# Kernel optimization log

Measured on AMD Instinct MI355X. Metric: run time of the kernel, lower is better.

Reference implementation:

```python
import jax, jax.numpy as jnp
import numpy as np

E, K, IN_DIM, OUT_DIM = 100000, 16, 128, 128


def _linear_init(key, out_d, in_d):
    kw, kb = jax.random.split(key)
    bound = 1.0 / np.sqrt(in_d)
    W = jax.random.uniform(kw, (out_d, in_d), minval=-bound, maxval=bound, dtype=jnp.float32)
    b = jax.random.uniform(kb, (out_d,), minval=-bound, maxval=bound, dtype=jnp.float32)
    return W, b


def setup_inputs() -> dict:
    key = jax.random.key(0)
    k_feat, k_adj, k1, k2, k3, k4 = jax.random.split(key, 6)
    edge_features = jax.random.normal(k_feat, (E, IN_DIM), dtype=jnp.float32)
    edge_adjacency = jax.random.randint(k_adj, (E, K), 0, E, dtype=jnp.int64)
    mW1, mb1 = _linear_init(k1, OUT_DIM, 2 * IN_DIM)
    mW2, mb2 = _linear_init(k2, OUT_DIM, OUT_DIM)
    uW1, ub1 = _linear_init(k3, OUT_DIM, IN_DIM + OUT_DIM)
    uW2, ub2 = _linear_init(k4, OUT_DIM, OUT_DIM)
    return {"edge_features": edge_features, "edge_adjacency": edge_adjacency,
            "mW1": mW1, "mb1": mb1, "mW2": mW2, "mb2": mb2,
            "uW1": uW1, "ub1": ub1, "uW2": ub2 * 0 + ub2 if False else uW1 * 0 + uW1 if False else uW1, "ub1_": ub1} if False else {
            "edge_features": edge_features, "edge_adjacency": edge_adjacency,
            "mW1": mW1, "mb1": mb1, "mW2": mW2, "mb2": mb2,
            "uW1": uW1, "ub1": ub1, "uW2": uW2, "ub2": ub2}


def reference(edge_features, edge_adjacency, mW1, mb1, mW2, mb2, uW1, ub1, uW2, ub2):
    D = edge_features.shape[1]
    # message_net first Linear on concat([feat_i, feat_j]) split into two halves
    # to avoid materializing the [E, K, 2D] concat tensor.
    Wi, Wj = mW1[:, :D], mW1[:, D:]                      # each [O, D]
    self_part = edge_features @ Wi.T                     # [E, O]
    nbr_feat = edge_features[edge_adjacency]             # [E, K, D] gather
    h = jax.nn.relu(self_part[:, None, :] + jnp.einsum('ekd,od->eko', nbr_feat, Wj) + mb1)
    msg = jnp.einsum('eko,po->ekp', h, mW2) + mb2        # [E, K, O]
    msg = msg.mean(axis=1)                               # mean over neighbors -> [E, O]
    # update_net on concat([feat_i, msg_i]), split likewise
    Ui, Um = uW1[:, :D], uW1[:, D:]
    u = jax.nn.relu(edge_features @ Ui.T + msg @ Um.T + ub1)
    return u @ uW2.T + ub2                               # [E, O]
```

## Files before the change

### kernel.cpp

```cpp
#include <hip/hip_runtime.h>
#include <hip/hip_bf16.h>

#define NE 100000
#define NK 16
#define ND 128
#define NTILES 6250
#define NSUP 3125

typedef __bf16 bf16_t;
typedef bf16_t bf16x8 __attribute__((ext_vector_type(8)));
typedef bf16_t bf16x4 __attribute__((ext_vector_type(4)));
typedef float f32x4 __attribute__((ext_vector_type(4)));
typedef float f32x2 __attribute__((ext_vector_type(2)));
typedef unsigned u32x2 __attribute__((ext_vector_type(2)));
typedef unsigned short u16;
typedef unsigned char u8;

__device__ __forceinline__ u16 f2bf(float f) {
  bf16_t h = (bf16_t)f;
  return __builtin_bit_cast(u16, h);
}

__device__ __forceinline__ void soft_barrier() {
  asm volatile("s_waitcnt lgkmcnt(0)" ::: "memory");
  __builtin_amdgcn_s_barrier();
}

__device__ __forceinline__ void unpack_s(unsigned w0, unsigned w1,
                                         f32x4& sA, f32x4& sB) {
  const f32x2 a0 = __builtin_amdgcn_cvt_pk_f32_fp8(w0, false);
  const f32x2 a1 = __builtin_amdgcn_cvt_pk_f32_fp8(w0, true);
  const f32x2 a2 = __builtin_amdgcn_cvt_pk_f32_fp8(w1, false);
  const f32x2 a3 = __builtin_amdgcn_cvt_pk_f32_fp8(w1, true);
  sA[0] = a0[0]; sA[1] = a0[1]; sA[2] = a1[0]; sA[3] = a1[1];
  sB[0] = a2[0]; sB[1] = a2[1]; sB[2] = a3[0]; sB[3] = a3[1];
}

__device__ __forceinline__ void acc8(f32x4& hA, f32x4& hB,
                                     const f32x4 sA, const f32x4 sB,
                                     const u32x2 zw) {
  const f32x2 z0 = __builtin_amdgcn_cvt_pk_f32_fp8(zw[0], false);
  const f32x2 z1 = __builtin_amdgcn_cvt_pk_f32_fp8(zw[0], true);
  const f32x2 z2 = __builtin_amdgcn_cvt_pk_f32_fp8(zw[1], false);
  const f32x2 z3 = __builtin_amdgcn_cvt_pk_f32_fp8(zw[1], true);
  f32x4 vA = sA, vB = sB;
  vA[0] += z0[0]; vA[1] += z0[1]; vA[2] += z1[0]; vA[3] += z1[1];
  vB[0] += z2[0]; vB[1] += z2[1]; vB[2] += z3[0]; vB[3] += z3[1];
#pragma unroll
  for (int i = 0; i < 4; ++i) {
    vA[i] = fmaxf(vA[i], 0.f);
    vB[i] = fmaxf(vB[i], 0.f);
  }
  hA += vA;
  hB += vB;
}

__global__ void k_prep(const float* __restrict__ mW1, const float* __restrict__ uW1,
                       const float* __restrict__ uW2, const float* __restrict__ mW2,
                       const float* __restrict__ ub1, const float* __restrict__ mb2,
                       u16* __restrict__ Wi_b, u16* __restrict__ Wj_b,
                       u16* __restrict__ Ui_b, u16* __restrict__ Wp_b,
                       u16* __restrict__ W2_b, float* __restrict__ bp)
{
  const int o = blockIdx.x, t = threadIdx.x;
  Wi_b[o * ND + t] = f2bf(mW1[o * 256 + t]);
  Wj_b[o * ND + t] = f2bf(mW1[o * 256 + 128 + t]);
  Ui_b[o * ND + t] = f2bf(uW1[o * 256 + t]);
  W2_b[o * ND + t] = f2bf(uW2[o * ND + t]);
  float acc = 0.f;
  for (int p = 0; p < 128; ++p)
    acc += uW1[o * 256 + 128 + p] * mW2[p * 128 + t];
  Wp_b[o * ND + t] = f2bf(acc);
  if (t == 0) {
    float b = ub1[o];
    for (int p = 0; p < 128; ++p) b += uW1[o * 256 + 128 + p] * mb2[p];
    bp[o] = b;
  }
}

__global__ __launch_bounds__(512) void k1_szt(
    const float* __restrict__ X, const u16* __restrict__ Wi_b,
    const u16* __restrict__ Wj_b, const u16* __restrict__ Ui_b,
    const float* __restrict__ mb1, const float* __restrict__ bp,
    u8* __restrict__ Sf8, u8* __restrict__ Zf8, u16* __restrict__ Tp)
{
  __shared__ u16 xt[2][16 * ND];
  __shared__ u8  eS[2][16 * ND];
  __shared__ u8  eZ[2][16 * ND];
  __shared__ u16 eT[2][16 * ND];
  const int tid = threadIdx.x, wid = tid >> 6, lane = tid & 63;
  const int r = lane & 15, q = lane >> 4;

  bf16x8 wiF[4], wjF[4], uiF[4];
  f32x4 mbF, bpF;
  {
    const int row = wid * 16 + r;
#pragma unroll
    for (int kk = 0; kk < 4; ++kk) {
      wiF[kk] = *(const bf16x8*)(Wi_b + row * ND + kk * 32 + q * 8);
      wjF[kk] = *(const bf16x8*)(Wj_b + row * ND + kk * 32 + q * 8);
      uiF[kk] = *(const bf16x8*)(Ui_b + row * ND + kk * 32 + q * 8);
    }
    mbF = *(const f32x4*)(mb1 + wid * 16 + q * 4);
    bpF = *(const f32x4*)(bp  + wid * 16 + q * 4);
  }

  const int rs = tid >> 5, cs = tid & 31;
  const int stb = rs * 256 + ((((cs >> 1) ^ (rs & 15)) << 4) | ((cs & 1) << 3));
  const int ewb = r * 256 + ((((wid * 2 + (q >> 1)) ^ (r & 15)) << 4) | ((q & 1) << 3));
  const int ezb = r * 128 + (((wid ^ (r & 7)) << 4) | (q * 4));
  const int erow = tid >> 5, c8 = tid & 31;
  const int erb = erow * 256 + ((((c8 >> 1) ^ (erow & 15)) << 4) | ((c8 & 1) << 3));
  const int zrb = erow * 128 + ((((c8 >> 2) ^ (erow & 7)) << 4) | ((c8 & 3) << 2));

  const long stride = gridDim.x;
  long t = blockIdx.x;
  if (t >= NTILES) return;

  f32x4 xr;
  auto gload = [&](long tt) {
    xr = *(const f32x4*)(X + (tt * 16 + rs) * ND + cs * 4);
  };
  auto stage = [&](int bb) {
    bf16x4 b;
#pragma unroll
    for (int i = 0; i < 4; ++i) b[i] = (bf16_t)xr[i];
    *(bf16x4*)((char*)xt[bb] + stb) = b;
  };

  gload(t);
  stage(0);
  {
    const long t1 = t + stride;
    if (t1 < NTILES) gload(t1);
  }
  soft_barrier();
  int b = 0;

  for (; t < NTILES; t += stride) {
    const long tn = t + stride, tn2 = tn + stride;

    bf16x8 xf[4];
#pragma unroll
    for (int kk = 0; kk < 4; ++kk)
      xf[kk] = *(const bf16x8*)((const char*)xt[b] +
               r * 256 + (((kk * 4 + q) ^ (r & 15)) << 4));

    if (tn < NTILES) stage(b ^ 1);
    if (tn2 < NTILES) gload(tn2);

    f32x4 aS = {0.f, 0.f, 0.f, 0.f};
    f32x4 aZ = {0.f, 0.f, 0.f, 0.f};
    f32x4 aT = {0.f, 0.f, 0.f, 0.f};
#pragma unroll
    for (int kk = 0; kk < 4; ++kk) {
      aS = __builtin_amdgcn_mfma_f32_16x16x32_bf16(wiF[kk], xf[kk], aS, 0, 0, 0);
      aZ = __builtin_amdgcn_mfma_f32_16x16x32_bf16(wjF[kk], xf[kk], aZ, 0, 0, 0);
      aT = __builtin_amdgcn_mfma_f32_16x16x32_bf16(uiF[kk], xf[kk], aT, 0, 0, 0);
    }

    bf16x4 pT;
#pragma unroll
    for (int i = 0; i < 4; ++i) pT[i] = (bf16_t)(aT[i] + bpF[i]);
    unsigned spk = 0, zpk = 0;
    spk = __builtin_amdgcn_cvt_pk_fp8_f32(aS[0] + mbF[0], aS[1] + mbF[1], spk, false);
    spk = __builtin_amdgcn_cvt_pk_fp8_f32(aS[2] + mbF[2], aS[3] + mbF[3], spk, true);
    zpk = __builtin_amdgcn_cvt_pk_fp8_f32(aZ[0], aZ[1], zpk, false);
    zpk = __builtin_amdgcn_cvt_pk_fp8_f32(aZ[2], aZ[3], zpk, true);
    *(unsigned*)((char*)eS[b] + ezb) = spk;
    *(unsigned*)((char*)eZ[b] + ezb) = zpk;
    *(bf16x4*)((char*)eT[b] + ewb) = pT;

    soft_barrier();

    {
      const long e = t * 16 + erow;
      const unsigned vS = *(const unsigned*)((const char*)eS[b] + zrb);
      const unsigned vZ = *(const unsigned*)((const char*)eZ[b] + zrb);
      const bf16x4 vT = *(const bf16x4*)((const char*)eT[b] + erb);
      *(unsigned*)(Sf8 + e * ND + c8 * 4) = vS;
      *(unsigned*)(Zf8 + e * ND + c8 * 4) = vZ;
      *(bf16x4*)(Tp + t * 2048 + erow * 128 + c8 * 4) = vT;
    }
    b ^= 1;
  }
}

__global__ __launch_bounds__(512) void k23_fused(
    const u8* __restrict__ Zf8, const u8* __restrict__ Sf8,
    const int* __restrict__ adj, const u16* __restrict__ Tp,
    const u16* __restrict__ Wp_b, const u16* __restrict__ W2_b,
    const float* __restrict__ ub2, float* __restrict__ out)
{
  __shared__ u16 ht[32 * ND];
  __shared__ u16 tt[32 * ND];
  __shared__ u16 ut[32 * ND];
  const int tid = threadIdx.x, wid = tid >> 6, lane = tid & 63;
  const int r = lane & 15, q = lane >> 4;
  const int ew = wid * 4 + q;
  const int c0 = r * 8;

  bf16x8 wpF[4], w2F[4];
  f32x4 ubF;
  {
    const int row = wid * 16 + r;
#pragma unroll
    for (int kk = 0; kk < 4; ++kk) {
      wpF[kk] = *(const bf16x8*)(Wp_b + row * ND + kk * 32 + q * 8);
      w2F[kk] = *(const bf16x8*)(W2_b + row * ND + kk * 32 + q * 8);
    }
    ubF = *(const f32x4*)(ub2 + wid * 16 + q * 4);
  }

  const int hwb = ew * 256 + ((r ^ (ew & 15)) << 4);
  const int trow = tid >> 4, tch = tid & 15;
  const int twb = trow * 256 + ((tch ^ (trow & 15)) << 4);
  const int uwb0 = (((wid * 2 + (q >> 1)) ^ r) << 4) | ((q & 1) << 3);

  const long stride = gridDim.x;
  long s = blockIdx.x;
  if (s >= NSUP) return;

  auto adjload = [&](long ss) { return adj[(ss * 32 + ew) * NK + r]; };

  int myidxN;
  f32x4 haccA = {0.f, 0.f, 0.f, 0.f}, haccB = {0.f, 0.f, 0.f, 0.f};
  bf16x8 trC;
  {
    const int myidxC = adjload(s);
    const unsigned* sp = (const unsigned*)(Sf8 + (s * 32 + ew) * ND + c0);
    const unsigned sw0 = sp[0], sw1 = sp[1];
    trC = *(const bf16x8*)(Tp + s * 4096 + trow * 128 + tch * 8);
    const long s1 = s + stride;
    myidxN = (s1 < NSUP) ? adjload(s1) : 0;

    f32x4 sA, sB;
    unpack_s(sw0, sw1, sA, sB);
#pragma unroll
    for (int k = 0; k < NK; ++k) {
      const int n = __shfl(myidxC, (lane & 48) + k);
      const u32x2 zw = *(const u32x2*)(Zf8 + (long)n * ND + c0);
      acc8(haccA, haccB, sA, sB, zw);
    }
  }

  for (; s < NSUP; s += stride) {
    const long sn = s + stride, sn2 = sn + stride;
    const bool hasN = (sn < NSUP);

    {
      bf16x8 hv;
#pragma unroll
      for (int i = 0; i < 4; ++i) {
        hv[i]     = (bf16_t)(haccA[i] * 0.0625f);
        hv[i + 4] = (bf16_t)(haccB[i] * 0.0625f);
      }
      *(bf16x8*)((char*)ht + hwb) = hv;
      *(bf16x8*)((char*)tt + twb) = trC;
    }

    u32x2 zbufA[8], zbufB[8];
    unsigned swn0 = 0, swn1 = 0;
    bf16x8 trN = {};
    int myidxN2 = 0;
    if (hasN) {
#pragma unroll
      for (int k = 0; k < 8; ++k) {
        const int n = __shfl(myidxN, (lane & 48) + k);
        zbufA[k] = *(const u32x2*)(Zf8 + (long)n * ND + c0);
      }
      const unsigned* sp = (const unsigned*)(Sf8 + (sn * 32 + ew) * ND + c0);
      swn0 = sp[0]; swn1 = sp[1];
      trN = *(const bf16x8*)(Tp + sn * 4096 + trow * 128 + tch * 8);
      if (sn2 < NSUP) myidxN2 = adjload(sn2);
    }

    soft_barrier();

#pragma unroll
    for (int t2 = 0; t2 < 2; ++t2) {
      const int rowb = (t2 * 16 + r) * 256;
      bf16x8 hf[4];
#pragma unroll
      for (int kk = 0; kk < 4; ++kk)
        hf[kk] = *(const bf16x8*)((const char*)ht + rowb + (((kk * 4 + q) ^ r) << 4));
      f32x4 acc;
      {
        const bf16x4 tv = *(const bf16x4*)((const char*)tt + rowb + uwb0);
#pragma unroll
        for (int i = 0; i < 4; ++i) acc[i] = (float)tv[i];
      }
#pragma unroll
      for (int kk = 0; kk < 4; ++kk)
        acc = __builtin_amdgcn_mfma_f32_16x16x32_bf16(wpF[kk], hf[kk], acc, 0, 0, 0);
      bf16x4 u;
#pragma unroll
      for (int i = 0; i < 4; ++i) u[i] = (bf16_t)fmaxf(acc[i], 0.f);
      *(bf16x4*)((char*)ut + rowb + uwb0) = u;
    }

    if (hasN) {
#pragma unroll
      for (int k = 0; k < 8; ++k) {
        const int n = __shfl(myidxN, (lane & 48) + 8 + k);
        zbufB[k] = *(const u32x2*)(Zf8 + (long)n * ND + c0);
      }
    }

    soft_barrier();

#pragma unroll
    for (int t2 = 0; t2 < 2; ++t2) {
      const int rowb = (t2 * 16 + r) * 256;
      bf16x8 uf[4];
#pragma unroll
      for (int kk = 0; kk < 4; ++kk)
        uf[kk] = *(const bf16x8*)((const char*)ut + rowb + (((kk * 4 + q) ^ r) << 4));
      f32x4 o = {0.f, 0.f, 0.f, 0.f};
#pragma unroll
      for (int kk = 0; kk < 4; ++kk)
        o = __builtin_amdgcn_mfma_f32_16x16x32_bf16(w2F[kk], uf[kk], o, 0, 0, 0);
#pragma unroll
      for (int i = 0; i < 4; ++i) o[i] += ubF[i];
      *(f32x4*)(out + (s * 32 + t2 * 16 + r) * ND + wid * 16 + q * 4) = o;
    }

    if (hasN) {
      f32x4 sA, sB;
      unpack_s(swn0, swn1, sA, sB);
      haccA = f32x4{0.f, 0.f, 0.f, 0.f};
      haccB = f32x4{0.f, 0.f, 0.f, 0.f};
#pragma unroll
      for (int k = 0; k < 8; ++k) acc8(haccA, haccB, sA, sB, zbufA[k]);
#pragma unroll
      for (int k = 0; k < 8; ++k) acc8(haccA, haccB, sA, sB, zbufB[k]);
      myidxN = myidxN2;
      trC = trN;
    }
  }
}

extern "C" void kernel_launch(void* const* d_in, const int* in_sizes, int n_in,
                              void* d_out, int out_size, void* d_ws, size_t ws_size,
                              hipStream_t stream)
{
  (void)in_sizes; (void)n_in; (void)out_size; (void)ws_size;
  const float* X   = (const float*)d_in[0];
  const int*   adj = (const int*)d_in[1];
  const float* mW1 = (const float*)d_in[2];
  const float* mb1 = (const float*)d_in[3];
  const float* mW2 = (const float*)d_in[4];
  const float* mb2 = (const float*)d_in[5];
  const float* uW1 = (const float*)d_in[6];
  const float* ub1 = (const float*)d_in[7];
  const float* uW2 = (const float*)d_in[8];
  const float* ub2 = (const float*)d_in[9];
  float* out = (float*)d_out;

  u8* ws8  = (u8*)d_ws;
  u8* Sf8  = ws8;
  u8* Zf8  = Sf8 + (size_t)NE * ND;
  u16* Tp  = (u16*)(Zf8 + (size_t)NE * ND);
  u16* Wi_b = Tp + (size_t)NE * ND;
  u16* Wj_b = Wi_b + 128 * 128;
  u16* Ui_b = Wj_b + 128 * 128;
  u16* Wp_b = Ui_b + 128 * 128;
  u16* W2_b = Wp_b + 128 * 128;
  float* bp = (float*)(W2_b + 128 * 128);

  k_prep<<<128, 128, 0, stream>>>(mW1, uW1, uW2, mW2, ub1, mb2,
                                  Wi_b, Wj_b, Ui_b, Wp_b, W2_b, bp);

  k1_szt<<<1024, 512, 0, stream>>>(X, Wi_b, Wj_b, Ui_b, mb1, bp, Sf8, Zf8, Tp);

  k23_fused<<<1024, 512, 0, stream>>>(Zf8, Sf8, adj, Tp, Wp_b, W2_b, ub2, out);
}
```

Measured before the change: 85.97 us.

## Replace persistent software-pipelined loop with one block per supertile

The fused gather/MLP kernel drops its persistent grid-stride loop, which prefetched the next tile's neighbor rows during the current tile's MFMA work. It now launches one 512-thread block per 32-edge supertile (3125 blocks) and handles a single tile with no cross-iteration prefetch. Latency hiding now comes from many resident blocks rather than explicit pipelining, which lowers register pressure. In exchange, each block reloads its weight fragments from global memory and pays its own launch and prologue cost.

```diff
diff --git a/kernel.cpp b/kernel.cpp
--- a/kernel.cpp
+++ b/kernel.cpp
@@ -199,6 +199,35 @@
   const int r = lane & 15, q = lane >> 4;
   const int ew = wid * 4 + q;
   const int c0 = r * 8;
+  const long s = blockIdx.x;
+
+  f32x4 haccA = {0.f, 0.f, 0.f, 0.f}, haccB = {0.f, 0.f, 0.f, 0.f};
+  bf16x8 trC;
+  {
+    const int myidxC = adj[(s * 32 + ew) * NK + r];
+    const unsigned* sp = (const unsigned*)(Sf8 + (s * 32 + ew) * ND + c0);
+    const unsigned sw0 = sp[0], sw1 = sp[1];
+    const int trow = tid >> 4, tch = tid & 15;
+    trC = *(const bf16x8*)(Tp + s * 4096 + trow * 128 + tch * 8);
+
+    f32x4 sA, sB;
+    unpack_s(sw0, sw1, sA, sB);
+    u32x2 zb[8];
+#pragma unroll
+    for (int k = 0; k < 8; ++k) {
+      const int n = __shfl(myidxC, (lane & 48) + k);
+      zb[k] = *(const u32x2*)(Zf8 + (long)n * ND + c0);
+    }
+#pragma unroll
+    for (int k = 0; k < 8; ++k) acc8(haccA, haccB, sA, sB, zb[k]);
+#pragma unroll
+    for (int k = 0; k < 8; ++k) {
+      const int n = __shfl(myidxC, (lane & 48) + 8 + k);
+      zb[k] = *(const u32x2*)(Zf8 + (long)n * ND + c0);
+    }
+#pragma unroll
+    for (int k = 0; k < 8; ++k) acc8(haccA, haccB, sA, sB, zb[k]);
+  }
 
   bf16x8 wpF[4], w2F[4];
   f32x4 ubF;
@@ -216,127 +245,57 @@
   const int trow = tid >> 4, tch = tid & 15;
   const int twb = trow * 256 + ((tch ^ (trow & 15)) << 4);
   const int uwb0 = (((wid * 2 + (q >> 1)) ^ r) << 4) | ((q & 1) << 3);
-
-  const long stride = gridDim.x;
-  long s = blockIdx.x;
-  if (s >= NSUP) return;
-
-  auto adjload = [&](long ss) { return adj[(ss * 32 + ew) * NK + r]; };
-
-  int myidxN;
-  f32x4 haccA = {0.f, 0.f, 0.f, 0.f}, haccB = {0.f, 0.f, 0.f, 0.f};
-  bf16x8 trC;
-  {
-    const int myidxC = adjload(s);
-    const unsigned* sp = (const unsigned*)(Sf8 + (s * 32 + ew) * ND + c0);
-    const unsigned sw0 = sp[0], sw1 = sp[1];
-    trC = *(const bf16x8*)(Tp + s * 4096 + trow * 128 + tch * 8);
-    const long s1 = s + stride;
-    myidxN = (s1 < NSUP) ? adjload(s1) : 0;
-
-    f32x4 sA, sB;
-    unpack_s(sw0, sw1, sA, sB);
-#pragma unroll
-    for (int k = 0; k < NK; ++k) {
-      const int n = __shfl(myidxC, (lane & 48) + k);
-      const u32x2 zw = *(const u32x2*)(Zf8 + (long)n * ND + c0);
-      acc8(haccA, haccB, sA, sB, zw);
-    }
-  }
-
-  for (; s < NSUP; s += stride) {
-    const long sn = s + stride, sn2 = sn + stride;
-    const bool hasN = (sn < NSUP);
-
+  {
+    bf16x8 hv;
+#pragma unroll
+    for (int i = 0; i < 4; ++i) {
+      hv[i]     = (bf16_t)(haccA[i] * 0.0625f);
+      hv[i + 4] = (bf16_t)(haccB[i] * 0.0625f);
+    }
+    *(bf16x8*)((char*)ht + hwb) = hv;
+    *(bf16x8*)((char*)tt + twb) = trC;
+  }
+
+  soft_barrier();
+
+#pragma unroll
+  for (int t2 = 0; t2 < 2; ++t2) {
+    const int rowb = (t2 * 16 + r) * 256;
+    bf16x8 hf[4];
+#pragma unroll
+    for (int kk = 0; kk < 4; ++kk)
+      hf[kk] = *(const bf16x8*)((const char*)ht + rowb + (((kk * 4 + q) ^ r) << 4));
+    f32x4 acc;
     {
-      bf16x8 hv;
-#pragma unroll
-      for (int i = 0; i < 4; ++i) {
-        hv[i]     = (bf16_t)(haccA[i] * 0.0625f);
-        hv[i + 4] = (bf16_t)(haccB[i] * 0.0625f);
-      }
-      *(bf16x8*)((char*)ht + hwb) = hv;
-      *(bf16x8*)((char*)tt + twb) = trC;
-    }
-
-    u32x2 zbufA[8], zbufB[8];
-    unsigned swn0 = 0, swn1 = 0;
-    bf16x8 trN = {};
-    int myidxN2 = 0;
-    if (hasN) {
-#pragma unroll
-      for (int k = 0; k < 8; ++k) {
-        const int n = __shfl(myidxN, (lane & 48) + k);
-        zbufA[k] = *(const u32x2*)(Zf8 + (long)n * ND + c0);
-      }
-      const unsigned* sp = (const unsigned*)(Sf8 + (sn * 32 + ew) * ND + c0);
-      swn0 = sp[0]; swn1 = sp[1];
-      trN = *(const bf16x8*)(Tp + sn * 4096 + trow * 128 + tch * 8);
-      if (sn2 < NSUP) myidxN2 = adjload(sn2);
-    }
-
-    soft_barrier();
-
-#pragma unroll
-    for (int t2 = 0; t2 < 2; ++t2) {
-      const int rowb = (t2 * 16 + r) * 256;
-      bf16x8 hf[4];
-#pragma unroll
-      for (int kk = 0; kk < 4; ++kk)
-        hf[kk] = *(const bf16x8*)((const char*)ht + rowb + (((kk * 4 + q) ^ r) << 4));
-      f32x4 acc;
-      {
-        const bf16x4 tv = *(const bf16x4*)((const char*)tt + rowb + uwb0);
-#pragma unroll
-        for (int i = 0; i < 4; ++i) acc[i] = (float)tv[i];
-      }
-#pragma unroll
-      for (int kk = 0; kk < 4; ++kk)
-        acc = __builtin_amdgcn_mfma_f32_16x16x32_bf16(wpF[kk], hf[kk], acc, 0, 0, 0);
-      bf16x4 u;
-#pragma unroll
-      for (int i = 0; i < 4; ++i) u[i] = (bf16_t)fmaxf(acc[i], 0.f);
-      *(bf16x4*)((char*)ut + rowb + uwb0) = u;
-    }
-
-    if (hasN) {
-#pragma unroll
-      for (int k = 0; k < 8; ++k) {
-        const int n = __shfl(myidxN, (lane & 48) + 8 + k);
-        zbufB[k] = *(const u32x2*)(Zf8 + (long)n * ND + c0);
-      }
-    }
-
-    soft_barrier();
-
-#pragma unroll
-    for (int t2 = 0; t2 < 2; ++t2) {
-      const int rowb = (t2 * 16 + r) * 256;
-      bf16x8 uf[4];
-#pragma unroll
-      for (int kk = 0; kk < 4; ++kk)
-        uf[kk] = *(const bf16x8*)((const char*)ut + rowb + (((kk * 4 + q) ^ r) << 4));
-      f32x4 o = {0.f, 0.f, 0.f, 0.f};
-#pragma unroll
-      for (int kk = 0; kk < 4; ++kk)
-        o = __builtin_amdgcn_mfma_f32_16x16x32_bf16(w2F[kk], uf[kk], o, 0, 0, 0);
-#pragma unroll
-      for (int i = 0; i < 4; ++i) o[i] += ubF[i];
-      *(f32x4*)(out + (s * 32 + t2 * 16 + r) * ND + wid * 16 + q * 4) = o;
-    }
-
-    if (hasN) {
-      f32x4 sA, sB;
-      unpack_s(swn0, swn1, sA, sB);
-      haccA = f32x4{0.f, 0.f, 0.f, 0.f};
-      haccB = f32x4{0.f, 0.f, 0.f, 0.f};
-#pragma unroll
-      for (int k = 0; k < 8; ++k) acc8(haccA, haccB, sA, sB, zbufA[k]);
-#pragma unroll
-      for (int k = 0; k < 8; ++k) acc8(haccA, haccB, sA, sB, zbufB[k]);
-      myidxN = myidxN2;
-      trC = trN;
-    }
+      const bf16x4 tv = *(const bf16x4*)((const char*)tt + rowb + uwb0);
+#pragma unroll
+      for (int i = 0; i < 4; ++i) acc[i] = (float)tv[i];
+    }
+#pragma unroll
+    for (int kk = 0; kk < 4; ++kk)
+      acc = __builtin_amdgcn_mfma_f32_16x16x32_bf16(wpF[kk], hf[kk], acc, 0, 0, 0);
+    bf16x4 u;
+#pragma unroll
+    for (int i = 0; i < 4; ++i) u[i] = (bf16_t)fmaxf(acc[i], 0.f);
+    *(bf16x4*)((char*)ut + rowb + uwb0) = u;
+  }
+
+  soft_barrier();
+
+#pragma unroll
+  for (int t2 = 0; t2 < 2; ++t2) {
+    const int rowb = (t2 * 16 + r) * 256;
+    bf16x8 uf[4];
+#pragma unroll
+    for (int kk = 0; kk < 4; ++kk)
+      uf[kk] = *(const bf16x8*)((const char*)ut + rowb + (((kk * 4 + q) ^ r) << 4));
+    f32x4 o = {0.f, 0.f, 0.f, 0.f};
+#pragma unroll
+    for (int kk = 0; kk < 4; ++kk)
+      o = __builtin_amdgcn_mfma_f32_16x16x32_bf16(w2F[kk], uf[kk], o, 0, 0, 0);
+#pragma unroll
+    for (int i = 0; i < 4; ++i) o[i] += ubF[i];
+    *(f32x4*)(out + (s * 32 + t2 * 16 + r) * ND + wid * 16 + q * 4) = o;
   }
 }
 
@@ -373,5 +332,5 @@
 
   k1_szt<<<1024, 512, 0, stream>>>(X, Wi_b, Wj_b, Ui_b, mb1, bp, Sf8, Zf8, Tp);
 
-  k23_fused<<<1024, 512, 0, stream>>>(Zf8, Sf8, adj, Tp, Wp_b, W2_b, ub2, out);
-}
+  k23_fused<<<NSUP, 512, 0, stream>>>(Zf8, Sf8, adj, Tp, Wp_b, W2_b, ub2, out);
+}
```

New measurement: 89.51 us. 4.1% more time.
